# Performance work log

Measured on AMD Instinct MI355X. Metric: run time of the kernel, lower is better.

Reference implementation:

```python
import jax, jax.numpy as jnp
import numpy as np

N_HEAD, D_K, D_V = 8, 256, 256
LN_EPS = 1e-6


def _positional_encoding(seq_len, d_model):
    # Faithful to PositionalEncoder: pe[pos, 2j]   = sin(pos / 10000**(2*(2j)/d))
    #                                pe[pos, 2j+1] = cos(pos / 10000**(2*(2j+1)/d))
    pos = jnp.arange(seq_len, dtype=jnp.float32)[:, None]          # [S,1]
    i = jnp.arange(0, d_model, 2, dtype=jnp.float32)               # even indices
    sin = jnp.sin(pos / jnp.power(10000.0, 2.0 * i / d_model))     # [S, d/2]
    cos = jnp.cos(pos / jnp.power(10000.0, 2.0 * (i + 1.0) / d_model))
    return jnp.stack([sin, cos], axis=-1).reshape(seq_len, d_model)


def setup_inputs() -> dict:
    key = jax.random.key(0)
    ks = jax.random.split(key, 6)
    b, n, h, w_half, c = 4, 8, 32, 16, 1024   # c == h*(2*w_half) required by rearrange
    d_emb = n * h * (2 * w_half)              # 8192 = n*h*w
    s = c                                     # token/seq length = 1024
    sc = 0.02
    return {
        "ref_img": jax.random.normal(ks[0], (b, n, h, w_half, c), jnp.float32),
        "hdmap": jax.random.normal(ks[1], (b, n, h, w_half, c), jnp.float32),
        "w_q": jax.random.normal(ks[2], (d_emb, N_HEAD * D_K), jnp.float32) * sc,
        "w_k": jax.random.normal(ks[3], (d_emb, N_HEAD * D_K), jnp.float32) * sc,
        "w_v": jax.random.normal(ks[4], (d_emb, N_HEAD * D_V), jnp.float32) * sc,
        "w_o": jax.random.normal(ks[5], (N_HEAD * D_V, d_emb), jnp.float32) * sc,
        "gamma": jnp.ones((s, d_emb), jnp.float32),
        "beta": jnp.zeros((s, d_emb), jnp.float32),
    }


def reference(ref_img, hdmap, w_q, w_k, w_v, w_o, gamma, beta):
    x = jnp.concatenate((ref_img, hdmap), axis=3)                  # [b,n,h,w,c]
    b, n, h, w, c = x.shape
    d = n * h * w                                                  # d_embedding
    # 'b n h w c -> b c (n h w)' : tokens = c, features = n*h*w
    x = jnp.transpose(x, (0, 4, 1, 2, 3)).reshape(b, c, d)
    x = x + 0.001 * _positional_encoding(c, d)[None]
    residual = x
    q = (x @ w_q).reshape(b, c, N_HEAD, D_K)
    k = (x @ w_k).reshape(b, c, N_HEAD, D_K)
    v = (x @ w_v).reshape(b, c, N_HEAD, D_V)
    scale = 1.0 / jnp.sqrt(jnp.float32(D_K))
    attn = jnp.einsum('bqhd,bkhd->bhqk', q * scale, k)             # [b,H,c,c]
    attn = jax.nn.softmax(attn, axis=-1)
    z = jnp.einsum('bhqk,bkhd->bqhd', attn, v).reshape(b, c, N_HEAD * D_V)
    z = z @ w_o + residual                                         # [b,c,d]
    # LayerNorm over last two dims ([seq_len, d_embedding])
    mean = jnp.mean(z, axis=(-2, -1), keepdims=True)
    var = jnp.var(z, axis=(-2, -1), keepdims=True)
    z = (z - mean) * jax.lax.rsqrt(var + LN_EPS) * gamma + beta
    # 'b (h w) (n c) -> b n c h w'
    z = z.reshape(b, h, w, n, c).transpose(0, 3, 4, 1, 2)
    return z
```

## Files before the change

kernel.cpp:

```cpp
#include <hip/hip_runtime.h>
#include <hip/hip_bf16.h>


typedef __attribute__((ext_vector_type(4))) float f32x4;
typedef __attribute__((ext_vector_type(8))) __bf16 bf16x8;
typedef __attribute__((ext_vector_type(8))) unsigned short ushort8;
typedef __attribute__((ext_vector_type(4))) unsigned short ushort4v;

static __device__ __forceinline__ float bf2f(unsigned short u) {
    unsigned int x = ((unsigned int)u) << 16;
    return __builtin_bit_cast(float, x);
}
static __device__ __forceinline__ unsigned short f2bf(float f) {
    unsigned int x = __builtin_bit_cast(unsigned int, f);
    unsigned int lsb = (x >> 16) & 1u;
    x += 0x7fffu + lsb;
    return (unsigned short)(x >> 16);
}

static __device__ __forceinline__ void gload16(const unsigned short* g, unsigned short* l) {
    __builtin_amdgcn_global_load_lds(
        (const __attribute__((address_space(1))) void*)g,
        (__attribute__((address_space(3))) void*)l,
        16, 0, 0);
}

__global__ __launch_bounds__(256) void build_x_kernel(
    const float* __restrict__ ref_img,
    const float* __restrict__ hdmap,
    unsigned short* __restrict__ x)
{
    __shared__ float tile[32][72];
    int slab = blockIdx.y;
    int b = slab >> 8;
    int n = (slab >> 5) & 7;
    int h = slab & 31;
    int t0 = blockIdx.x * 64;
    int tid = threadIdx.x;

    {
        int w  = tid >> 3;
        int tg = tid & 7;
        const float* src = (w < 16)
            ? ref_img + ((size_t)(((b * 8 + n) * 32 + h) * 16 + w) * 1024 + t0 + tg * 8)
            : hdmap   + ((size_t)(((b * 8 + n) * 32 + h) * 16 + (w - 16)) * 1024 + t0 + tg * 8);
        *(f32x4*)&tile[w][tg * 8]     = *(const f32x4*)src;
        *(f32x4*)&tile[w][tg * 8 + 4] = *(const f32x4*)(src + 4);
    }
    __syncthreads();
    {
        int tau = tid >> 2;
        int wg  = tid & 3;
        int t = t0 + tau;
        const float L = 13.287712379549449f;
        ushort8 o;
        #pragma unroll
        for (int e = 0; e < 8; ++e) {
            int w = wg * 8 + e;
            int f = n * 1024 + h * 32 + w;
            int j = f >> 1;
            float ex = ((f & 1) ? (4.0f * (float)j + 2.0f) : (4.0f * (float)j)) * (1.0f / 8192.0f);
            float freq = exp2f(-ex * L);
            float arg = (float)t * freq;
            float pe = (f & 1) ? cosf(arg) : sinf(arg);
            o[e] = f2bf(tile[w][tau] + 0.001f * pe);
        }
        unsigned short* dst = x + ((size_t)(b * 1024 + t)) * 8192 + n * 1024 + h * 32 + wg * 8;
        *(ushort8*)dst = o;
    }
}

__global__ __launch_bounds__(256) void wconv_kernel(
    const float* __restrict__ w, unsigned short* __restrict__ wt, int K, int N)
{
    __shared__ unsigned short tile[64][72];
    int k0 = blockIdx.x * 64, n0 = blockIdx.y * 64;
    int tid = threadIdx.x;
    {
        int kl = tid >> 4;
        int nl = (tid & 15) * 4;
        #pragma unroll
        for (int i = 0; i < 4; ++i) {
            f32x4 v = *(const f32x4*)(w + (long)(k0 + kl + i * 16) * N + n0 + nl);
            tile[kl + i * 16][nl + 0] = f2bf(v[0]);
            tile[kl + i * 16][nl + 1] = f2bf(v[1]);
            tile[kl + i * 16][nl + 2] = f2bf(v[2]);
            tile[kl + i * 16][nl + 3] = f2bf(v[3]);
        }
    }
    __syncthreads();
    {
        int nl = tid >> 2;
        int kg = (tid & 3) * 16;
        ushort8 o0, o1;
        #pragma unroll
        for (int e = 0; e < 8; ++e) { o0[e] = tile[kg + e][nl]; o1[e] = tile[kg + 8 + e][nl]; }
        unsigned short* dst = wt + (long)(n0 + nl) * K + k0 + kg;
        *(ushort8*)dst = o0;
        *(ushort8*)(dst + 8) = o1;
    }
}

template<int OUT_F32, int RESID, int STORE_TRANS>
__global__ __launch_bounds__(256) void gemm_kernel(
    const unsigned short* __restrict__ A, const unsigned short* __restrict__ B,
    void* __restrict__ Cp, const unsigned short* __restrict__ resid,
    int K, int lda, int ldb, int ldc,
    long sA2, long sB2, long sC2, float alpha)
{
    __shared__ unsigned short As[128 * 32];
    __shared__ unsigned short Bs[128 * 32];

    int z = blockIdx.z;
    const unsigned short* Ab = A + (long)z * sA2;
    const unsigned short* Bb = B + (long)z * sB2;
    long coff = (long)z * sC2;

    int bm = blockIdx.y * 128, bn = blockIdx.x * 128;
    int tid = threadIdx.x;
    int lane = tid & 63;
    int wave = tid >> 6;
    int wm = (wave >> 1) * 64, wn = (wave & 1) * 64;
    int l15 = lane & 15, quad = lane >> 4;

    int c1 = tid + 256;
    int r0 = tid >> 2, g0 = (tid & 3) * 8;
    int r1 = c1 >> 2,  g1 = (c1 & 3) * 8;

    const unsigned short* a0p = Ab + (long)(bm + r0) * lda + g0;
    const unsigned short* a1p = Ab + (long)(bm + r1) * lda + g1;
    const unsigned short* b0p = Bb + (long)(bn + r0) * ldb + g0;
    const unsigned short* b1p = Bb + (long)(bn + r1) * ldb + g1;
    unsigned short* al0 = As + tid * 8;
    unsigned short* al1 = As + c1 * 8;
    unsigned short* bl0 = Bs + tid * 8;
    unsigned short* bl1 = Bs + c1 * 8;

    f32x4 acc[4][4] = {};

    for (int k0 = 0; k0 < K; k0 += 32) {
        gload16(a0p + k0, al0);
        gload16(a1p + k0, al1);
        gload16(b0p + k0, bl0);
        gload16(b1p + k0, bl1);
        __syncthreads();

        bf16x8 af[4], bfv[4];
        #pragma unroll
        for (int mi = 0; mi < 4; ++mi)
            af[mi] = *(const bf16x8*)&As[(wm + mi * 16 + l15) * 32 + quad * 8];
        #pragma unroll
        for (int ni = 0; ni < 4; ++ni)
            bfv[ni] = *(const bf16x8*)&Bs[(wn + ni * 16 + l15) * 32 + quad * 8];
        #pragma unroll
        for (int mi = 0; mi < 4; ++mi)
            #pragma unroll
            for (int ni = 0; ni < 4; ++ni)
                acc[mi][ni] = __builtin_amdgcn_mfma_f32_16x16x32_bf16(
                    af[mi], bfv[ni], acc[mi][ni], 0, 0, 0);
        __syncthreads();
    }

    if (STORE_TRANS) {
        unsigned short* vt = (unsigned short*)Cp;
        #pragma unroll
        for (int mi = 0; mi < 4; ++mi) {
            #pragma unroll
            for (int ni = 0; ni < 4; ++ni) {
                int row = bm + wm + mi * 16 + quad * 4;
                int col = bn + wn + ni * 16 + l15;
                ushort4v o;
                #pragma unroll
                for (int r = 0; r < 4; ++r) o[r] = f2bf(acc[mi][ni][r] * alpha);
                *(ushort4v*)(vt + (long)(row >> 10) * 2097152
                                + (long)col * 1024 + (row & 1023)) = o;
            }
        }
    } else {
        #pragma unroll
        for (int mi = 0; mi < 4; ++mi)
            #pragma unroll
            for (int ni = 0; ni < 4; ++ni)
                #pragma unroll
                for (int r = 0; r < 4; ++r) {
                    int row = bm + wm + mi * 16 + quad * 4 + r;
                    int col = bn + wn + ni * 16 + l15;
                    float v = acc[mi][ni][r] * alpha;
                    long ci = coff + (long)row * ldc + col;
                    if (RESID) v += bf2f(resid[ci]);
                    if (OUT_F32) ((float*)Cp)[ci] = v;
                    else         ((unsigned short*)Cp)[ci] = f2bf(v);
                }
    }
}

__global__ __launch_bounds__(256) void softmax_kernel(float* __restrict__ s)
{
    long row = blockIdx.x;
    float* p = s + row * 1024;
    unsigned short* dst = (unsigned short*)s + row * 2048;
    int tid = threadIdx.x;
    int lane = tid & 63, wv = tid >> 6;

    f32x4 v = *(const f32x4*)(p + tid * 4);
    float m = fmaxf(fmaxf(v[0], v[1]), fmaxf(v[2], v[3]));
    #pragma unroll
    for (int off = 32; off; off >>= 1) m = fmaxf(m, __shfl_xor(m, off, 64));
    __shared__ float redm[4];
    if (lane == 0) redm[wv] = m;
    __syncthreads();
    m = fmaxf(fmaxf(redm[0], redm[1]), fmaxf(redm[2], redm[3]));

    f32x4 e;
    e[0] = __expf(v[0] - m); e[1] = __expf(v[1] - m);
    e[2] = __expf(v[2] - m); e[3] = __expf(v[3] - m);
    float sum = e[0] + e[1] + e[2] + e[3];
    #pragma unroll
    for (int off = 32; off; off >>= 1) sum += __shfl_xor(sum, off, 64);
    __shared__ float reds[4];
    if (lane == 0) reds[wv] = sum;
    __syncthreads();
    sum = reds[0] + reds[1] + reds[2] + reds[3];

    float inv = 1.0f / sum;
    ushort4v o;
    o[0] = f2bf(e[0] * inv); o[1] = f2bf(e[1] * inv);
    o[2] = f2bf(e[2] * inv); o[3] = f2bf(e[3] * inv);
    *(ushort4v*)(dst + tid * 4) = o;
}

__global__ __launch_bounds__(256) void ln_stats_kernel(
    const unsigned short* __restrict__ zo, float* __restrict__ stats)
{
    int b = blockIdx.y;
    const ushort8* p = (const ushort8*)(zo + (long)b * 8388608);
    float s = 0.f, sq = 0.f;
    for (int i = blockIdx.x * 256 + threadIdx.x; i < 1048576; i += 128 * 256) {
        ushort8 u = p[i];
        #pragma unroll
        for (int e = 0; e < 8; ++e) {
            float f = bf2f(u[e]);
            s += f; sq += f * f;
        }
    }
    #pragma unroll
    for (int off = 32; off; off >>= 1) {
        s += __shfl_xor(s, off, 64);
        sq += __shfl_xor(sq, off, 64);
    }
    __shared__ float rs[4], rq[4];
    int lane = threadIdx.x & 63, wv = threadIdx.x >> 6;
    if (lane == 0) { rs[wv] = s; rq[wv] = sq; }
    __syncthreads();
    if (threadIdx.x == 0) {
        atomicAdd(&stats[b * 2 + 0], rs[0] + rs[1] + rs[2] + rs[3]);
        atomicAdd(&stats[b * 2 + 1], rq[0] + rq[1] + rq[2] + rq[3]);
    }
}

__global__ __launch_bounds__(256) void ln_apply_kernel(
    const unsigned short* __restrict__ zo,
    const float* __restrict__ gamma,
    const float* __restrict__ beta,
    const float* __restrict__ stats,
    float* __restrict__ out)
{
    __shared__ float tile[64][65];
    int b = blockIdx.z, t0 = blockIdx.y * 64, f0 = blockIdx.x * 64;
    float mean = stats[b * 2 + 0] * (1.0f / 8388608.0f);
    float var  = stats[b * 2 + 1] * (1.0f / 8388608.0f) - mean * mean;
    float rstd = rsqrtf(var + 1e-6f);
    int tid = threadIdx.x;

    #pragma unroll
    for (int i = 0; i < 4; ++i) {
        int rt = (tid >> 4) + i * 16;
        int c4 = (tid & 15) * 4;
        long zi = (long)b * 8388608 + (long)(t0 + rt) * 8192 + f0 + c4;
        ushort4v zv = *(const ushort4v*)(zo + zi);
        long gi = (long)(t0 + rt) * 8192 + f0 + c4;
        f32x4 g  = *(const f32x4*)(gamma + gi);
        f32x4 bt = *(const f32x4*)(beta + gi);
        #pragma unroll
        for (int e = 0; e < 4; ++e)
            tile[rt][c4 + e] = (bf2f(zv[e]) - mean) * rstd * g[e] + bt[e];
    }
    __syncthreads();

    int fl = tid >> 2;
    int tg = tid & 3;
    int f = f0 + fl;
    int np = f >> 10, cp = f & 1023;
    long obase = ((long)((b * 8 + np) * 1024 + cp)) * 1024 + t0 + tg * 16;
    #pragma unroll
    for (int c = 0; c < 4; ++c) {
        f32x4 o;
        #pragma unroll
        for (int e = 0; e < 4; ++e) o[e] = tile[tg * 16 + c * 4 + e][fl];
        *(f32x4*)(out + obase + c * 4) = o;
    }
}

extern "C" void kernel_launch(void* const* d_in, const int* in_sizes, int n_in,
                              void* d_out, int out_size, void* d_ws, size_t ws_size,
                              hipStream_t stream)
{
    const float* ref_img = (const float*)d_in[0];
    const float* hdmap   = (const float*)d_in[1];
    const float* w_q     = (const float*)d_in[2];
    const float* w_k     = (const float*)d_in[3];
    const float* w_v     = (const float*)d_in[4];
    const float* w_o     = (const float*)d_in[5];
    const float* gamma   = (const float*)d_in[6];
    const float* beta    = (const float*)d_in[7];

    char* ws = (char*)d_ws;
    const size_t MB = 1024 * 1024;
    unsigned short* x  = (unsigned short*)(ws);
    unsigned short* q  = (unsigned short*)(ws + 64 * MB);
    unsigned short* k  = (unsigned short*)(ws + 80 * MB);
    unsigned short* vT = (unsigned short*)(ws + 96 * MB);
    unsigned short* wT = (unsigned short*)(ws + 112 * MB);
    float* sc          = (float*)(ws + 112 * MB);
    float* stats       = (float*)(ws + 144 * MB);
    unsigned short* z2 = q;
    unsigned short* zo = x;

    hipMemsetAsync(stats, 0, 32, stream);

    build_x_kernel<<<dim3(16, 1024), 256, 0, stream>>>(ref_img, hdmap, x);

    wconv_kernel<<<dim3(128, 32), 256, 0, stream>>>(w_q, wT, 8192, 2048);
    gemm_kernel<0,0,0><<<dim3(16, 32, 1), 256, 0, stream>>>(
        x, wT, q, nullptr, 8192, 8192, 8192, 2048, 0, 0, 0, 1.0f);

    wconv_kernel<<<dim3(128, 32), 256, 0, stream>>>(w_k, wT, 8192, 2048);
    gemm_kernel<0,0,0><<<dim3(16, 32, 1), 256, 0, stream>>>(
        x, wT, k, nullptr, 8192, 8192, 8192, 2048, 0, 0, 0, 1.0f);

    wconv_kernel<<<dim3(128, 32), 256, 0, stream>>>(w_v, wT, 8192, 2048);
    gemm_kernel<0,0,1><<<dim3(16, 32, 1), 256, 0, stream>>>(
        x, wT, vT, nullptr, 8192, 8192, 8192, 0, 0, 0, 0, 1.0f);

    for (int b = 0; b < 4; ++b) {
        long o2 = (long)b * 2097152;
        gemm_kernel<1,0,0><<<dim3(8, 8, 8), 256, 0, stream>>>(
            q + o2, k + o2, sc, nullptr,
            256, 2048, 2048, 1024, 256L, 256L, 1048576L, 0.0625f);
        softmax_kernel<<<8192, 256, 0, stream>>>(sc);
        gemm_kernel<0,0,0><<<dim3(2, 8, 8), 256, 0, stream>>>(
            (const unsigned short*)sc, vT + o2, z2 + o2, nullptr,
            1024, 2048, 1024, 2048, 2097152L, 262144L, 256L, 1.0f);
    }

    wconv_kernel<<<dim3(32, 128), 256, 0, stream>>>(w_o, wT, 2048, 8192);
    gemm_kernel<0,1,0><<<dim3(64, 32, 1), 256, 0, stream>>>(
        z2, wT, zo, x, 2048, 2048, 2048, 8192, 0, 0, 0, 1.0f);

    ln_stats_kernel<<<dim3(128, 4), 256, 0, stream>>>(zo, stats);
    ln_apply_kernel<<<dim3(128, 16, 4), 256, 0, stream>>>(
        zo, gamma, beta, stats, (float*)d_out);
}
```

Baseline: 1.584 ms.

## Add 256x256 double-buffered GEMM kernel for QKV and output projections

Adds a new 512-thread GEMM with 256x256 tiles, 64-wide K steps, double-buffered LDS with async global-to-LDS prefetch interleaved between MFMA phases, swizzled LDS offsets to avoid bank conflicts, XCD-aware block remapping and s_setprio around MFMA bursts. The large projection GEMMs (QKV and output) switch to it, while the attention GEMMs keep the old 128x128 kernel. The goal is more data reuse per tile and overlap of memory loads with compute in the original synchronous loop. It uses a large LDS footprint (128KB per block) and depends on hand-tuned vmcnt waits being correct.

New measurement: 1.495 ms. -5.6%, faster.

```diff
diff --git a/kernel.cpp b/kernel.cpp
--- a/kernel.cpp
+++ b/kernel.cpp
@@ -101,70 +101,136 @@
     }
 }
 
-template<int OUT_F32, int RESID, int STORE_TRANS>
-__global__ __launch_bounds__(256) void gemm_kernel(
+template<int RESID, int STORE_TRANS>
+__global__ __launch_bounds__(512, 2) void gemm256_kernel(
     const unsigned short* __restrict__ A, const unsigned short* __restrict__ B,
     void* __restrict__ Cp, const unsigned short* __restrict__ resid,
-    int K, int lda, int ldb, int ldc,
-    long sA2, long sB2, long sC2, float alpha)
-{
-    __shared__ unsigned short As[128 * 32];
-    __shared__ unsigned short Bs[128 * 32];
-
-    int z = blockIdx.z;
-    const unsigned short* Ab = A + (long)z * sA2;
-    const unsigned short* Bb = B + (long)z * sB2;
-    long coff = (long)z * sC2;
-
-    int bm = blockIdx.y * 128, bn = blockIdx.x * 128;
+    int K, int lda, int ldb, int ldc, float alpha)
+{
+    __shared__ unsigned short lds[2][4][8192];
+
+    int nwg = gridDim.x * gridDim.y;
+    int flat = blockIdx.y * gridDim.x + blockIdx.x;
+    int qq = nwg >> 3, rr = nwg & 7;
+    int xcd = flat & 7, idx = flat >> 3;
+    int sid = (xcd < rr ? xcd * (qq + 1) : rr * (qq + 1) + (xcd - rr) * qq) + idx;
+    int bx = sid % gridDim.x, by = sid / gridDim.x;
+    int bm = by * 256, bn = bx * 256;
+
     int tid = threadIdx.x;
-    int lane = tid & 63;
-    int wave = tid >> 6;
-    int wm = (wave >> 1) * 64, wn = (wave & 1) * 64;
+    int lane = tid & 63, wave = tid >> 6;
     int l15 = lane & 15, quad = lane >> 4;
-
-    int c1 = tid + 256;
-    int r0 = tid >> 2, g0 = (tid & 3) * 8;
-    int r1 = c1 >> 2,  g1 = (c1 & 3) * 8;
-
-    const unsigned short* a0p = Ab + (long)(bm + r0) * lda + g0;
-    const unsigned short* a1p = Ab + (long)(bm + r1) * lda + g1;
-    const unsigned short* b0p = Bb + (long)(bn + r0) * ldb + g0;
-    const unsigned short* b1p = Bb + (long)(bn + r1) * ldb + g1;
-    unsigned short* al0 = As + tid * 8;
-    unsigned short* al1 = As + c1 * 8;
-    unsigned short* bl0 = Bs + tid * 8;
-    unsigned short* bl1 = Bs + c1 * 8;
-
-    f32x4 acc[4][4] = {};
-
-    for (int k0 = 0; k0 < K; k0 += 32) {
-        gload16(a0p + k0, al0);
-        gload16(a1p + k0, al1);
-        gload16(b0p + k0, bl0);
-        gload16(b1p + k0, bl1);
-        __syncthreads();
-
-        bf16x8 af[4], bfv[4];
-        #pragma unroll
-        for (int mi = 0; mi < 4; ++mi)
-            af[mi] = *(const bf16x8*)&As[(wm + mi * 16 + l15) * 32 + quad * 8];
-        #pragma unroll
-        for (int ni = 0; ni < 4; ++ni)
-            bfv[ni] = *(const bf16x8*)&Bs[(wn + ni * 16 + l15) * 32 + quad * 8];
+    int wm = (wave >> 2) * 128;
+    int wn = (wave & 3) * 64;
+
+    int offA[8], offB[4];
+    #pragma unroll
+    for (int mi = 0; mi < 8; ++mi) {
+        int r = wm + mi * 16 + l15;
+        offA[mi] = r * 32 + (((quad + (r >> 1)) & 3) << 3);
+    }
+    #pragma unroll
+    for (int ni = 0; ni < 4; ++ni) {
+        int c = wn + ni * 16 + l15;
+        offB[ni] = c * 32 + (((quad + (c >> 1)) & 3) << 3);
+    }
+
+    int row0 = tid >> 2;
+    int ls   = ((tid & 3) - (row0 >> 1)) & 3;
+    long a0 = (long)(bm + row0) * lda + ls * 8;
+    long a1 = a0 + 128L * lda;
+    long b0 = (long)(bn + row0) * ldb + ls * 8;
+    long b1 = b0 + 128L * ldb;
+    int d0 = tid * 8, d1 = tid * 8 + 4096;
+
+    f32x4 acc[8][4] = {};
+    int nt = K >> 6;
+
+    gload16(A + a0, &lds[0][0][d0]); gload16(A + a1, &lds[0][0][d1]);
+    gload16(B + b0, &lds[0][2][d0]); gload16(B + b1, &lds[0][2][d1]);
+    gload16(A + a0 + 32, &lds[0][1][d0]); gload16(A + a1 + 32, &lds[0][1][d1]);
+    gload16(B + b0 + 32, &lds[0][3][d0]); gload16(B + b1 + 32, &lds[0][3][d1]);
+    asm volatile("s_waitcnt vmcnt(4)" ::: "memory");
+    __builtin_amdgcn_s_barrier();
+
+    for (int t = 0; t < nt; ++t) {
+        int cur = t & 1, nxt = cur ^ 1;
+        long kn = (long)(t + 1) * 64;
+        bool pf = (t + 1 < nt);
+        bf16x8 af[4], bf[4];
+
+        #pragma unroll
+        for (int mi = 0; mi < 4; ++mi) af[mi] = *(const bf16x8*)&lds[cur][0][offA[mi]];
+        #pragma unroll
+        for (int ni = 0; ni < 4; ++ni) bf[ni] = *(const bf16x8*)&lds[cur][2][offB[ni]];
+        if (pf) { gload16(A + a0 + kn, &lds[nxt][0][d0]);
+                  gload16(A + a1 + kn, &lds[nxt][0][d1]); }
+        __builtin_amdgcn_s_barrier();
+        __builtin_amdgcn_s_setprio(1);
         #pragma unroll
         for (int mi = 0; mi < 4; ++mi)
             #pragma unroll
             for (int ni = 0; ni < 4; ++ni)
                 acc[mi][ni] = __builtin_amdgcn_mfma_f32_16x16x32_bf16(
-                    af[mi], bfv[ni], acc[mi][ni], 0, 0, 0);
-        __syncthreads();
+                    af[mi], bf[ni], acc[mi][ni], 0, 0, 0);
+        __builtin_amdgcn_s_setprio(0);
+        __builtin_amdgcn_s_barrier();
+
+        #pragma unroll
+        for (int mi = 0; mi < 4; ++mi) af[mi] = *(const bf16x8*)&lds[cur][0][offA[mi + 4]];
+        if (pf) { gload16(B + b0 + kn, &lds[nxt][2][d0]);
+                  gload16(B + b1 + kn, &lds[nxt][2][d1]); }
+        if (pf) asm volatile("s_waitcnt vmcnt(4)" ::: "memory");
+        else    asm volatile("s_waitcnt vmcnt(0)" ::: "memory");
+        __builtin_amdgcn_s_barrier();
+        __builtin_amdgcn_s_setprio(1);
+        #pragma unroll
+        for (int mi = 0; mi < 4; ++mi)
+            #pragma unroll
+            for (int ni = 0; ni < 4; ++ni)
+                acc[mi + 4][ni] = __builtin_amdgcn_mfma_f32_16x16x32_bf16(
+                    af[mi], bf[ni], acc[mi + 4][ni], 0, 0, 0);
+        __builtin_amdgcn_s_setprio(0);
+        __builtin_amdgcn_s_barrier();
+
+        #pragma unroll
+        for (int mi = 0; mi < 4; ++mi) af[mi] = *(const bf16x8*)&lds[cur][1][offA[mi]];
+        #pragma unroll
+        for (int ni = 0; ni < 4; ++ni) bf[ni] = *(const bf16x8*)&lds[cur][3][offB[ni]];
+        if (pf) { gload16(A + a0 + kn + 32, &lds[nxt][1][d0]);
+                  gload16(A + a1 + kn + 32, &lds[nxt][1][d1]); }
+        __builtin_amdgcn_s_barrier();
+        __builtin_amdgcn_s_setprio(1);
+        #pragma unroll
+        for (int mi = 0; mi < 4; ++mi)
+            #pragma unroll
+            for (int ni = 0; ni < 4; ++ni)
+                acc[mi][ni] = __builtin_amdgcn_mfma_f32_16x16x32_bf16(
+                    af[mi], bf[ni], acc[mi][ni], 0, 0, 0);
+        __builtin_amdgcn_s_setprio(0);
+        __builtin_amdgcn_s_barrier();
+
+        #pragma unroll
+        for (int mi = 0; mi < 4; ++mi) af[mi] = *(const bf16x8*)&lds[cur][1][offA[mi + 4]];
+        if (pf) { gload16(B + b0 + kn + 32, &lds[nxt][3][d0]);
+                  gload16(B + b1 + kn + 32, &lds[nxt][3][d1]); }
+        if (pf) asm volatile("s_waitcnt vmcnt(4)" ::: "memory");
+        __builtin_amdgcn_s_barrier();
+        __builtin_amdgcn_s_setprio(1);
+        #pragma unroll
+        for (int mi = 0; mi < 4; ++mi)
+            #pragma unroll
+            for (int ni = 0; ni < 4; ++ni)
+                acc[mi + 4][ni] = __builtin_amdgcn_mfma_f32_16x16x32_bf16(
+                    af[mi], bf[ni], acc[mi + 4][ni], 0, 0, 0);
+        __builtin_amdgcn_s_setprio(0);
+        __builtin_amdgcn_s_barrier();
     }
 
     if (STORE_TRANS) {
         unsigned short* vt = (unsigned short*)Cp;
         #pragma unroll
-        for (int mi = 0; mi < 4; ++mi) {
+        for (int mi = 0; mi < 8; ++mi) {
             #pragma unroll
             for (int ni = 0; ni < 4; ++ni) {
                 int row = bm + wm + mi * 16 + quad * 4;
@@ -178,6 +244,98 @@
         }
     } else {
         #pragma unroll
+        for (int mi = 0; mi < 8; ++mi)
+            #pragma unroll
+            for (int ni = 0; ni < 4; ++ni)
+                #pragma unroll
+                for (int r = 0; r < 4; ++r) {
+                    int row = bm + wm + mi * 16 + quad * 4 + r;
+                    int col = bn + wn + ni * 16 + l15;
+                    float v = acc[mi][ni][r] * alpha;
+                    long ci = (long)row * ldc + col;
+                    if (RESID) v += bf2f(resid[ci]);
+                    ((unsigned short*)Cp)[ci] = f2bf(v);
+                }
+    }
+}
+
+template<int OUT_F32, int RESID, int STORE_TRANS>
+__global__ __launch_bounds__(256) void gemm_kernel(
+    const unsigned short* __restrict__ A, const unsigned short* __restrict__ B,
+    void* __restrict__ Cp, const unsigned short* __restrict__ resid,
+    int K, int lda, int ldb, int ldc,
+    long sA2, long sB2, long sC2, float alpha)
+{
+    __shared__ unsigned short As[128 * 32];
+    __shared__ unsigned short Bs[128 * 32];
+
+    int z = blockIdx.z;
+    const unsigned short* Ab = A + (long)z * sA2;
+    const unsigned short* Bb = B + (long)z * sB2;
+    long coff = (long)z * sC2;
+
+    int bm = blockIdx.y * 128, bn = blockIdx.x * 128;
+    int tid = threadIdx.x;
+    int lane = tid & 63;
+    int wave = tid >> 6;
+    int wm = (wave >> 1) * 64, wn = (wave & 1) * 64;
+    int l15 = lane & 15, quad = lane >> 4;
+
+    int c1 = tid + 256;
+    int r0 = tid >> 2, g0 = (tid & 3) * 8;
+    int r1 = c1 >> 2,  g1 = (c1 & 3) * 8;
+
+    const unsigned short* a0p = Ab + (long)(bm + r0) * lda + g0;
+    const unsigned short* a1p = Ab + (long)(bm + r1) * lda + g1;
+    const unsigned short* b0p = Bb + (long)(bn + r0) * ldb + g0;
+    const unsigned short* b1p = Bb + (long)(bn + r1) * ldb + g1;
+    unsigned short* al0 = As + tid * 8;
+    unsigned short* al1 = As + c1 * 8;
+    unsigned short* bl0 = Bs + tid * 8;
+    unsigned short* bl1 = Bs + c1 * 8;
+
+    f32x4 acc[4][4] = {};
+
+    for (int k0 = 0; k0 < K; k0 += 32) {
+        gload16(a0p + k0, al0);
+        gload16(a1p + k0, al1);
+        gload16(b0p + k0, bl0);
+        gload16(b1p + k0, bl1);
+        __syncthreads();
+
+        bf16x8 af[4], bfv[4];
+        #pragma unroll
+        for (int mi = 0; mi < 4; ++mi)
+            af[mi] = *(const bf16x8*)&As[(wm + mi * 16 + l15) * 32 + quad * 8];
+        #pragma unroll
+        for (int ni = 0; ni < 4; ++ni)
+            bfv[ni] = *(const bf16x8*)&Bs[(wn + ni * 16 + l15) * 32 + quad * 8];
+        #pragma unroll
+        for (int mi = 0; mi < 4; ++mi)
+            #pragma unroll
+            for (int ni = 0; ni < 4; ++ni)
+                acc[mi][ni] = __builtin_amdgcn_mfma_f32_16x16x32_bf16(
+                    af[mi], bfv[ni], acc[mi][ni], 0, 0, 0);
+        __syncthreads();
+    }
+
+    if (STORE_TRANS) {
+        unsigned short* vt = (unsigned short*)Cp;
+        #pragma unroll
+        for (int mi = 0; mi < 4; ++mi) {
+            #pragma unroll
+            for (int ni = 0; ni < 4; ++ni) {
+                int row = bm + wm + mi * 16 + quad * 4;
+                int col = bn + wn + ni * 16 + l15;
+                ushort4v o;
+                #pragma unroll
+                for (int r = 0; r < 4; ++r) o[r] = f2bf(acc[mi][ni][r] * alpha);
+                *(ushort4v*)(vt + (long)(row >> 10) * 2097152
+                                + (long)col * 1024 + (row & 1023)) = o;
+            }
+        }
+    } else {
+        #pragma unroll
         for (int mi = 0; mi < 4; ++mi)
             #pragma unroll
             for (int ni = 0; ni < 4; ++ni)
@@ -331,16 +489,16 @@
     build_x_kernel<<<dim3(16, 1024), 256, 0, stream>>>(ref_img, hdmap, x);
 
     wconv_kernel<<<dim3(128, 32), 256, 0, stream>>>(w_q, wT, 8192, 2048);
-    gemm_kernel<0,0,0><<<dim3(16, 32, 1), 256, 0, stream>>>(
-        x, wT, q, nullptr, 8192, 8192, 8192, 2048, 0, 0, 0, 1.0f);
+    gemm256_kernel<0,0><<<dim3(8, 16), 512, 0, stream>>>(
+        x, wT, q, nullptr, 8192, 8192, 8192, 2048, 1.0f);
 
     wconv_kernel<<<dim3(128, 32), 256, 0, stream>>>(w_k, wT, 8192, 2048);
-    gemm_kernel<0,0,0><<<dim3(16, 32, 1), 256, 0, stream>>>(
-        x, wT, k, nullptr, 8192, 8192, 8192, 2048, 0, 0, 0, 1.0f);
+    gemm256_kernel<0,0><<<dim3(8, 16), 512, 0, stream>>>(
+        x, wT, k, nullptr, 8192, 8192, 8192, 2048, 1.0f);
 
     wconv_kernel<<<dim3(128, 32), 256, 0, stream>>>(w_v, wT, 8192, 2048);
-    gemm_kernel<0,0,1><<<dim3(16, 32, 1), 256, 0, stream>>>(
-        x, wT, vT, nullptr, 8192, 8192, 8192, 0, 0, 0, 0, 1.0f);
+    gemm256_kernel<0,1><<<dim3(8, 16), 512, 0, stream>>>(
+        x, wT, vT, nullptr, 8192, 8192, 8192, 0, 1.0f);
 
     for (int b = 0; b < 4; ++b) {
         long o2 = (long)b * 2097152;
@@ -354,8 +512,8 @@
     }
 
     wconv_kernel<<<dim3(32, 128), 256, 0, stream>>>(w_o, wT, 2048, 8192);
-    gemm_kernel<0,1,0><<<dim3(64, 32, 1), 256, 0, stream>>>(
-        z2, wT, zo, x, 2048, 2048, 2048, 8192, 0, 0, 0, 1.0f);
+    gemm256_kernel<1,0><<<dim3(32, 16), 512, 0, stream>>>(
+        z2, wT, zo, x, 2048, 2048, 2048, 8192, 1.0f);
 
     ln_stats_kernel<<<dim3(128, 4), 256, 0, stream>>>(zo, stats);
     ln_apply_kernel<<<dim3(128, 16, 4), 256, 0, stream>>>(
```
